# Kernel tuning notes

Hardware: AMD Instinct MI355X
Metric: run time of the kernel (lower is better)

## Reference

```python
import jax, jax.numpy as jnp
import numpy as np


def _shift(x, axis, d):
    # value at voxel p becomes x[p + d*e_axis], zero outside the grid
    n = x.shape[axis]
    zero = jnp.zeros_like(jax.lax.slice_in_dim(x, 0, 1, axis=axis))
    if d > 0:
        return jnp.concatenate([jax.lax.slice_in_dim(x, 1, n, axis=axis), zero], axis=axis)
    return jnp.concatenate([zero, jax.lax.slice_in_dim(x, 0, n - 1, axis=axis)], axis=axis)


def _forward(coords, instance_gt, S, num_scales):
    # InputLayer mode=4: average features of duplicate coords.
    # features = [instance+1, 1]; averaging duplicates of [v,1] gives [mean(v), 1].
    inst = instance_gt.astype(jnp.float32) + 1.0
    c = coords.astype(jnp.int32)
    flat = (c[:, 0] * S + c[:, 1]) * S + c[:, 2]
    ssum = jnp.zeros(S * S * S, jnp.float32).at[flat].add(inst)
    cnt = jnp.zeros(S * S * S, jnp.float32).at[flat].add(1.0)
    val = (ssum / jnp.maximum(cnt, 1.0)).reshape(S, S, S)   # mean label per active voxel, 0 if inactive
    act = (cnt > 0).astype(jnp.float32).reshape(S, S, S)    # active-site mask
    outs = []
    for scale in range(num_scales):
        if scale == 0:
            v, a = val, act
        else:
            f = 2 ** scale
            Ss = S // f
            # scn AveragePooling divides by pool volume; features[:, :1]/count then
            # renormalizes -> mean of val over ACTIVE fine voxels in the block.
            vsum = val.reshape(Ss, f, Ss, f, Ss, f).sum(axis=(1, 3, 5))
            asum = act.reshape(Ss, f, Ss, f, Ss, f).sum(axis=(1, 3, 5))
            a = (asum > 0).astype(jnp.float32)
            v = vsum / jnp.maximum(asum, 1.0)
        va = v * a
        feats = []
        masks = []
        # one-hot submanifold conv kernel offsets (4,22,10,16,12,14) = (-x,+x,-y,+y,-z,+z)
        for axis in range(3):
            for d in (-1, 1):
                sh = _shift(va, axis, d)                      # neighbor value, 0 if neighbor inactive
                feats.append((jnp.abs(sh - v) < 0.01).astype(jnp.float32))
                masks.append((sh > 0).astype(jnp.float32))
        # submanifold conv is only defined at active sites -> mask by a
        out = jnp.stack(feats + masks, axis=-1) * a[..., None]  # [Ss,Ss,Ss,12]
        outs.append(out.reshape(-1, 12))
    return jnp.concatenate(outs, axis=0)


def setup_inputs() -> dict:
    key = jax.random.key(0)
    k1, k2 = jax.random.split(key)
    N, S = 4_000_000, 128
    coords = jax.random.randint(k1, (N, 3), 0, S, dtype=jnp.int32)
    instance_gt = jax.random.randint(k2, (N,), 0, 50).astype(jnp.float32)
    return {"coords": coords, "instance_gt": instance_gt, "inputScale": S, "numScales": 6}


def reference(coords, instance_gt, inputScale, numScales):
    return _forward(coords, instance_gt, inputScale, numScales)
```

## Files before the change

kernel.cpp:

```cpp
#include <hip/hip_runtime.h>

#define GS3 2097152
#define NS1 262144
#define NS2 32768
#define NS3 4096
#define NS4 512
#define NS5 64
#define NSALL 299584

#define OB1 25165824
#define OB2 28311552
#define OB3 28704768
#define OB4 28753920
#define OB5 28760064

#define NREG 512
#define RVOX 4096
#define PPB  8192
#define RPT  (PPB / 256)
#define CAPB 64


__global__ __launch_bounds__(256) void bin_kernel(
    const int* __restrict__ coords, const float* __restrict__ inst,
    unsigned int* __restrict__ counts, unsigned int* __restrict__ bins, int N) {
  __shared__ unsigned srec[PPB];
  __shared__ unsigned hist[NREG];
  __shared__ unsigned lofs[NREG];
  __shared__ unsigned part[256];
  __shared__ unsigned total_sh;
  unsigned vrec[RPT];
  int tid = threadIdx.x;
  int bid = blockIdx.x;
  int start = bid * PPB;
  for (int j = tid; j < NREG; j += 256) hist[j] = 0;
  __syncthreads();
#pragma unroll
  for (int j = 0; j < RPT; j++) {
    int i = start + j * 256 + tid;
    unsigned v = 0xFFFFFFFFu;
    if (i < N) {
      int x = coords[3 * i + 0];
      int y = coords[3 * i + 1];
      int z = coords[3 * i + 2];
      unsigned lab = (unsigned)inst[i] + 1u;
      unsigned r = (((unsigned)x >> 1) << 3) | ((unsigned)y >> 4);
      unsigned l = (((unsigned)x & 1) << 11) | (((unsigned)y & 15) << 7) | (unsigned)z;
      v = (r << 18) | (l << 6) | lab;
      atomicAdd(&hist[r], 1u);
    }
    vrec[j] = v;
  }
  __syncthreads();
  unsigned ha = hist[2 * tid], hb = hist[2 * tid + 1];
  counts[(size_t)bid * NREG + 2 * tid]     = ha < CAPB ? ha : CAPB;
  counts[(size_t)bid * NREG + 2 * tid + 1] = hb < CAPB ? hb : CAPB;
  part[tid] = ha + hb;
  __syncthreads();
  for (int o = 1; o < 256; o <<= 1) {
    unsigned v = part[tid];
    unsigned add = (tid >= o) ? part[tid - o] : 0u;
    __syncthreads();
    part[tid] = v + add;
    __syncthreads();
  }
  unsigned inc = part[tid];
  unsigned ex = inc - (ha + hb);
  lofs[2 * tid] = ex;
  lofs[2 * tid + 1] = ex + ha;
  if (tid == 255) total_sh = inc;
  __syncthreads();
  for (int j = tid; j < NREG; j += 256) hist[j] = 0;
  __syncthreads();
#pragma unroll
  for (int j = 0; j < RPT; j++) {
    unsigned v = vrec[j];
    if (v != 0xFFFFFFFFu) {
      unsigned r = v >> 18;
      unsigned pos = lofs[r] + atomicAdd(&hist[r], 1u);
      srec[pos] = v;
    }
  }
  __syncthreads();
  unsigned total = total_sh;
  size_t bbase = (size_t)bid * NREG * CAPB;
  for (unsigned j = tid; j < total; j += 256) {
    unsigned v = srec[j];
    unsigned r = v >> 18;
    unsigned p = j - lofs[r];
    if (p < CAPB) bins[bbase + r * CAPB + p] = v & 0x3FFFFu;
  }
}

__global__ __launch_bounds__(256) void build_pool_kernel(
    const unsigned int* __restrict__ counts, const unsigned int* __restrict__ bins,
    unsigned int* __restrict__ P,
    double* __restrict__ vs1, double* __restrict__ as1, int nchunks) {
  __shared__ unsigned grid[RVOX];
  int r = blockIdx.x;
  int tid = threadIdx.x;
  for (int j = tid; j < RVOX; j += 256) grid[j] = 0;
  __syncthreads();
  for (int b = tid; b < nchunks; b += 256) {
    int cb = (int)counts[(size_t)b * NREG + r];
    const unsigned* src = bins + ((size_t)b * NREG + r) * CAPB;
    for (int k = 0; k < cb; k++) {
      unsigned v = src[k];
      atomicAdd(&grid[v >> 6], (1u << 20) | (v & 63u));
    }
  }
  __syncthreads();
  int X = r >> 3, yo = r & 7;
  unsigned pbase = ((unsigned)(2 * X) << 14) | ((unsigned)yo << 11);
  for (int j = tid; j < RVOX; j += 256) {
    P[pbase + ((j >> 11) << 14) + (j & 0x7FF)] = grid[j];
  }
  for (int c = tid; c < 512; c += 256) {
    int yl = c >> 6, Z = c & 63;
    double vs = 0.0, as = 0.0;
#pragma unroll
    for (int dx = 0; dx < 2; dx++)
#pragma unroll
      for (int dy = 0; dy < 2; dy++)
#pragma unroll
        for (int dz = 0; dz < 2; dz++) {
          int j = (dx << 11) | ((2 * yl + dy) << 7) | (2 * Z + dz);
          unsigned pk = grid[j];
          unsigned cc = pk >> 20;
          if (cc) {
            vs += (double)(pk & 0xFFFFFu) / (double)cc;
            as += 1.0;
          }
        }
    int q = (X << 12) | (((yo << 3) + yl) << 6) | Z;
    vs1[q] = vs;
    as1[q] = as;
  }
}

__global__ __launch_bounds__(256) void poolRest_kernel(
    const double* __restrict__ vs1, const double* __restrict__ as1,
    double* __restrict__ vs2, double* __restrict__ as2,
    double* __restrict__ vs3, double* __restrict__ as3,
    double* __restrict__ vs4, double* __restrict__ as4,
    double* __restrict__ vs5, double* __restrict__ as5) {
  int t = blockIdx.x * blockDim.x + threadIdx.x;

  if (t < NS2) {
    int q = t;
    int X = q >> 10, Y = (q >> 5) & 31, Z = q & 31;
    double vs = 0.0, as = 0.0;
#pragma unroll
    for (int dx = 0; dx < 2; dx++)
#pragma unroll
      for (int dy = 0; dy < 2; dy++)
#pragma unroll
        for (int dz = 0; dz < 2; dz++) {
          int p = ((((X << 1) + dx) << 12) + (((Y << 1) + dy) << 6) + ((Z << 1) + dz));
          vs += vs1[p];
          as += as1[p];
        }
    vs2[q] = vs;
    as2[q] = as;
    return;
  }
  t -= NS2;
  if (t < NS3) {
    int q = t;
    int X = q >> 8, Y = (q >> 4) & 15, Z = q & 15;
    double vs = 0.0, as = 0.0;
    for (int dx = 0; dx < 4; dx++)
      for (int dy = 0; dy < 4; dy++)
#pragma unroll
        for (int dz = 0; dz < 4; dz++) {
          int p = ((((X << 2) + dx) << 12) + (((Y << 2) + dy) << 6) + ((Z << 2) + dz));
          vs += vs1[p];
          as += as1[p];
        }
    vs3[q] = vs;
    as3[q] = as;
    return;
  }
  t -= NS3;
  if (t < NS4 * 64) {
    int w = t >> 6, lane = t & 63;
    int X = w >> 6, Y = (w >> 3) & 7, Z = w & 7;
    double vs = 0.0, as = 0.0;
#pragma unroll
    for (int j = 0; j < 8; j++) {
      int c = lane * 8 + j;
      int dx = c >> 6, dy = (c >> 3) & 7, dz = c & 7;
      int p = ((((X << 3) + dx) << 12) + (((Y << 3) + dy) << 6) + ((Z << 3) + dz));
      vs += vs1[p];
      as += as1[p];
    }
    for (int o = 32; o > 0; o >>= 1) {
      vs += __shfl_down(vs, o, 64);
      as += __shfl_down(as, o, 64);
    }
    if (lane == 0) { vs4[w] = vs; as4[w] = as; }
    return;
  }
  t -= NS4 * 64;
  if (t < NS5 * 64) {
    int w = t >> 6, lane = t & 63;
    int X = w >> 4, Y = (w >> 2) & 3, Z = w & 3;
    double vs = 0.0, as = 0.0;
    for (int j = 0; j < 64; j++) {
      int c = lane * 64 + j;
      int dx = c >> 8, dy = (c >> 4) & 15, dz = c & 15;
      int p = ((((X << 4) + dx) << 12) + (((Y << 4) + dy) << 6) + ((Z << 4) + dz));
      vs += vs1[p];
      as += as1[p];
    }
    for (int o = 32; o > 0; o >>= 1) {
      vs += __shfl_down(vs, o, 64);
      as += __shfl_down(as, o, 64);
    }
    if (lane == 0) { vs5[w] = vs; as5[w] = as; }
  }
}

__global__ __launch_bounds__(256) void out_kernel(
    const unsigned int* __restrict__ P,
    const double* __restrict__ vs1, const double* __restrict__ as1,
    const double* __restrict__ vs2, const double* __restrict__ as2,
    const double* __restrict__ vs3, const double* __restrict__ as3,
    const double* __restrict__ vs4, const double* __restrict__ as4,
    const double* __restrict__ vs5, const double* __restrict__ as5,
    float* __restrict__ out) {
  int p = blockIdx.x * blockDim.x + threadIdx.x;
  if (p < GS3) {
    unsigned pk = P[p];
    int cc = (int)(pk >> 20);
    float4 r0 = {0.f, 0.f, 0.f, 0.f}, r1 = r0, r2 = r0;
    if (cc) {
      int sc = (int)(pk & 0xFFFFFu);
      int x = p >> 14, y = (p >> 7) & 127, z = p & 127;
      const int off[6] = {-(1 << 14), (1 << 14), -(1 << 7), (1 << 7), -1, 1};
      const bool inb[6] = {x > 0, x < 127, y > 0, y < 127, z > 0, z < 127};
      float f[6], m[6];
#pragma unroll
      for (int k = 0; k < 6; k++) {
        int sn = 0, cn = 0;
        if (inb[k]) {
          unsigned pn = P[p + off[k]];
          cn = (int)(pn >> 20);
          sn = (int)(pn & 0xFFFFFu);
        }
        if (cn) {
          long long d = (long long)sn * cc - (long long)sc * cn;
          if (d < 0) d = -d;
          f[k] = (100ll * d < (long long)cn * cc) ? 1.f : 0.f;
          m[k] = 1.f;
        } else {
          f[k] = 0.f;
          m[k] = 0.f;
        }
      }
      r0 = {f[0], f[1], f[2], f[3]};
      r1 = {f[4], f[5], m[0], m[1]};
      r2 = {m[2], m[3], m[4], m[5]};
    }
    float4* o = (float4*)(out + 12ll * p);
    o[0] = r0; o[1] = r1; o[2] = r2;
    return;
  }
  int t = p - GS3;
  const double *vs, *as;
  int ls, q;
  long long obase;
  if (t < NS1) { q = t; vs = vs1; as = as1; ls = 6; obase = OB1; }
  else if (t < NS1 + NS2) { q = t - NS1; vs = vs2; as = as2; ls = 5; obase = OB2; }
  else if (t < NS1 + NS2 + NS3) { q = t - NS1 - NS2; vs = vs3; as = as3; ls = 4; obase = OB3; }
  else if (t < NS1 + NS2 + NS3 + NS4) { q = t - NS1 - NS2 - NS3; vs = vs4; as = as4; ls = 3; obase = OB4; }
  else if (t < NSALL) { q = t - NS1 - NS2 - NS3 - NS4; vs = vs5; as = as5; ls = 2; obase = OB5; }
  else return;

  int Ss = 1 << ls;
  int X = q >> (2 * ls), Y = (q >> ls) & (Ss - 1), Z = q & (Ss - 1);
  double ac = as[q];
  float4 r0 = {0.f, 0.f, 0.f, 0.f}, r1 = r0, r2 = r0;
  if (ac > 0.0) {
    double vc = vs[q] / ac;
    const int off[6] = {-(Ss * Ss), Ss * Ss, -Ss, Ss, -1, 1};
    const bool inb[6] = {X > 0, X < Ss - 1, Y > 0, Y < Ss - 1, Z > 0, Z < Ss - 1};
    float f[6], m[6];
#pragma unroll
    for (int k = 0; k < 6; k++) {
      double van = 0.0;
      if (inb[k]) {
        double an = as[q + off[k]];
        if (an > 0.0) van = vs[q + off[k]] / an;
      }
      f[k] = (fabs(van - vc) < 0.01) ? 1.f : 0.f;
      m[k] = (van > 0.0) ? 1.f : 0.f;
    }
    r0 = {f[0], f[1], f[2], f[3]};
    r1 = {f[4], f[5], m[0], m[1]};
    r2 = {m[2], m[3], m[4], m[5]};
  }
  float4* o = (float4*)(out + obase + 12ll * q);
  o[0] = r0; o[1] = r1; o[2] = r2;
}

extern "C" void kernel_launch(void* const* d_in, const int* in_sizes, int n_in,
                              void* d_out, int out_size, void* d_ws, size_t ws_size,
                              hipStream_t stream) {
  const int* coords = (const int*)d_in[0];
  const float* inst = (const float*)d_in[1];
  int N = in_sizes[1];
  float* out = (float*)d_out;
  int nchunks = (N + PPB - 1) / PPB;

  char* base = (char*)d_ws;
  unsigned int* P = (unsigned int*)base;
  double* vs1 = (double*)(base + 8388608);
  double* as1 = vs1 + NS1;
  double* vs2 = as1 + NS1; double* as2 = vs2 + NS2;
  double* vs3 = as2 + NS2; double* as3 = vs3 + NS3;
  double* vs4 = as3 + NS3; double* as4 = vs4 + NS4;
  double* vs5 = as4 + NS4; double* as5 = vs5 + NS5;
  size_t counts_off = 13182976;
  unsigned int* counts = (unsigned int*)(base + counts_off);
  size_t bins_off = counts_off + ((size_t)nchunks * NREG * 4 + 1023) / 1024 * 1024;
  unsigned int* bins = (unsigned int*)(base + bins_off);
  size_t need = bins_off + (size_t)nchunks * NREG * CAPB * 4;
  if (ws_size < need) return;

  bin_kernel<<<nchunks, 256, 0, stream>>>(coords, inst, counts, bins, N);
  build_pool_kernel<<<NREG, 256, 0, stream>>>(counts, bins, P, vs1, as1, nchunks);
  poolRest_kernel<<<(NS2 + NS3 + NS4 * 64 + NS5 * 64 + 255) / 256, 256, 0, stream>>>(
      vs1, as1, vs2, as2, vs3, as3, vs4, as4, vs5, as5);
  out_kernel<<<(GS3 + NSALL + 255) / 256, 256, 0, stream>>>(
      P, vs1, as1, vs2, as2, vs3, as3, vs4, as4, vs5, as5, out);
}
```

Before: 86.41 us.

## Fuse coarse pooling scales into output kernel, recomputing neighbor block sums

Drops the separate poolRest kernel and the intermediate vs2..vs5 buffers. Each coarse-scale output thread, or wave for the two coarsest scales, now sums the scale-1 pooled values for its own block and its six neighbors, then writes the 12 features directly. This removes one kernel launch and a global round trip. In exchange every pooled block is reduced up to seven times, which is extra reads of vs1/as1 and longer per-thread loops at scales 2 and 3.

After: 159.0 us. +84.0%, slower.

```diff
diff --git a/kernel.cpp b/kernel.cpp
--- a/kernel.cpp
+++ b/kernel.cpp
@@ -6,7 +6,6 @@
 #define NS3 4096
 #define NS4 512
 #define NS5 64
-#define NSALL 299584
 
 #define OB1 25165824
 #define OB2 28311552
@@ -19,6 +18,13 @@
 #define PPB  8192
 #define RPT  (PPB / 256)
 #define CAPB 64
+
+#define T1 (GS3)
+#define T2 (T1 + NS1)
+#define T3 (T2 + NS2)
+#define T4 (T3 + NS3)
+#define T5 (T4 + NS4 * 64)
+#define TEND (T5 + NS5 * 64)
 
 
 __global__ __launch_bounds__(256) void bin_kernel(
@@ -138,96 +144,104 @@
   }
 }
 
-__global__ __launch_bounds__(256) void poolRest_kernel(
+__device__ __forceinline__ void writeOut12(float* dst, const float* f, const float* m) {
+  float4 r0 = {f[0], f[1], f[2], f[3]};
+  float4 r1 = {f[4], f[5], m[0], m[1]};
+  float4 r2 = {m[2], m[3], m[4], m[5]};
+  float4* o = (float4*)dst;
+  o[0] = r0; o[1] = r1; o[2] = r2;
+}
+
+__device__ __forceinline__ void coarse_thread(
     const double* __restrict__ vs1, const double* __restrict__ as1,
-    double* __restrict__ vs2, double* __restrict__ as2,
-    double* __restrict__ vs3, double* __restrict__ as3,
-    double* __restrict__ vs4, double* __restrict__ as4,
-    double* __restrict__ vs5, double* __restrict__ as5) {
-  int t = blockIdx.x * blockDim.x + threadIdx.x;
-
-  if (t < NS2) {
-    int q = t;
-    int X = q >> 10, Y = (q >> 5) & 31, Z = q & 31;
-    double vs = 0.0, as = 0.0;
-#pragma unroll
-    for (int dx = 0; dx < 2; dx++)
-#pragma unroll
-      for (int dy = 0; dy < 2; dy++)
-#pragma unroll
-        for (int dz = 0; dz < 2; dz++) {
-          int p = ((((X << 1) + dx) << 12) + (((Y << 1) + dy) << 6) + ((Z << 1) + dz));
-          vs += vs1[p];
-          as += as1[p];
-        }
-    vs2[q] = vs;
-    as2[q] = as;
-    return;
-  }
-  t -= NS2;
-  if (t < NS3) {
-    int q = t;
-    int X = q >> 8, Y = (q >> 4) & 15, Z = q & 15;
-    double vs = 0.0, as = 0.0;
-    for (int dx = 0; dx < 4; dx++)
-      for (int dy = 0; dy < 4; dy++)
-#pragma unroll
-        for (int dz = 0; dz < 4; dz++) {
-          int p = ((((X << 2) + dx) << 12) + (((Y << 2) + dy) << 6) + ((Z << 2) + dz));
-          vs += vs1[p];
-          as += as1[p];
-        }
-    vs3[q] = vs;
-    as3[q] = as;
-    return;
-  }
-  t -= NS3;
-  if (t < NS4 * 64) {
-    int w = t >> 6, lane = t & 63;
-    int X = w >> 6, Y = (w >> 3) & 7, Z = w & 7;
-    double vs = 0.0, as = 0.0;
-#pragma unroll
-    for (int j = 0; j < 8; j++) {
-      int c = lane * 8 + j;
-      int dx = c >> 6, dy = (c >> 3) & 7, dz = c & 7;
-      int p = ((((X << 3) + dx) << 12) + (((Y << 3) + dy) << 6) + ((Z << 3) + dz));
-      vs += vs1[p];
-      as += as1[p];
-    }
+    float* __restrict__ out, int q, int lg, int lc, long long obase) {
+  int G = 1 << lg, C = 1 << lc;
+  int X = q >> (2 * lg), Y = (q >> lg) & (G - 1), Z = q & (G - 1);
+  const int cx[7] = {X, X - 1, X + 1, X, X, X, X};
+  const int cy[7] = {Y, Y, Y, Y - 1, Y + 1, Y, Y};
+  const int cz[7] = {Z, Z, Z, Z, Z, Z - 1, Z + 1};
+  double vsum[7], asum[7];
+#pragma unroll
+  for (int c = 0; c < 7; c++) {
+    vsum[c] = 0.0; asum[c] = 0.0;
+    if (cx[c] < 0 || cx[c] >= G || cy[c] < 0 || cy[c] >= G || cz[c] < 0 || cz[c] >= G)
+      continue;
+    int bx = cx[c] << lc, by = cy[c] << lc, bz = cz[c] << lc;
+    for (int dx = 0; dx < C; dx++)
+      for (int dy = 0; dy < C; dy++)
+        for (int dz = 0; dz < C; dz++) {
+          int p1 = ((bx + dx) << 12) | ((by + dy) << 6) | (bz + dz);
+          vsum[c] += vs1[p1];
+          asum[c] += as1[p1];
+        }
+  }
+  float f[6], m[6];
+  if (asum[0] > 0.0) {
+    double vc = vsum[0] / asum[0];
+#pragma unroll
+    for (int k = 0; k < 6; k++) {
+      double van = (asum[k + 1] > 0.0) ? vsum[k + 1] / asum[k + 1] : 0.0;
+      f[k] = (fabs(van - vc) < 0.01) ? 1.f : 0.f;
+      m[k] = (van > 0.0) ? 1.f : 0.f;
+    }
+  } else {
+#pragma unroll
+    for (int k = 0; k < 6; k++) { f[k] = 0.f; m[k] = 0.f; }
+  }
+  writeOut12(out + obase + 12ll * q, f, m);
+}
+
+__device__ __forceinline__ void coarse_wave(
+    const double* __restrict__ vs1, const double* __restrict__ as1,
+    float* __restrict__ out, int t, int lg, int lc, long long obase) {
+  int w = t >> 6, lane = t & 63;
+  int G = 1 << lg, C = 1 << lc, vol = C * C * C;
+  int X = w >> (2 * lg), Y = (w >> lg) & (G - 1), Z = w & (G - 1);
+  const int cx[7] = {X, X - 1, X + 1, X, X, X, X};
+  const int cy[7] = {Y, Y, Y, Y - 1, Y + 1, Y, Y};
+  const int cz[7] = {Z, Z, Z, Z, Z, Z - 1, Z + 1};
+  double vsum[7], asum[7];
+#pragma unroll
+  for (int c = 0; c < 7; c++) {
+    vsum[c] = 0.0; asum[c] = 0.0;
+    if (cx[c] < 0 || cx[c] >= G || cy[c] < 0 || cy[c] >= G || cz[c] < 0 || cz[c] >= G)
+      continue;
+    int bx = cx[c] << lc, by = cy[c] << lc, bz = cz[c] << lc;
+    for (int ch = lane; ch < vol; ch += 64) {
+      int dx = ch >> (2 * lc), dy = (ch >> lc) & (C - 1), dz = ch & (C - 1);
+      int p1 = ((bx + dx) << 12) | ((by + dy) << 6) | (bz + dz);
+      vsum[c] += vs1[p1];
+      asum[c] += as1[p1];
+    }
+  }
+#pragma unroll
+  for (int c = 0; c < 7; c++) {
     for (int o = 32; o > 0; o >>= 1) {
-      vs += __shfl_down(vs, o, 64);
-      as += __shfl_down(as, o, 64);
-    }
-    if (lane == 0) { vs4[w] = vs; as4[w] = as; }
-    return;
-  }
-  t -= NS4 * 64;
-  if (t < NS5 * 64) {
-    int w = t >> 6, lane = t & 63;
-    int X = w >> 4, Y = (w >> 2) & 3, Z = w & 3;
-    double vs = 0.0, as = 0.0;
-    for (int j = 0; j < 64; j++) {
-      int c = lane * 64 + j;
-      int dx = c >> 8, dy = (c >> 4) & 15, dz = c & 15;
-      int p = ((((X << 4) + dx) << 12) + (((Y << 4) + dy) << 6) + ((Z << 4) + dz));
-      vs += vs1[p];
-      as += as1[p];
-    }
-    for (int o = 32; o > 0; o >>= 1) {
-      vs += __shfl_down(vs, o, 64);
-      as += __shfl_down(as, o, 64);
-    }
-    if (lane == 0) { vs5[w] = vs; as5[w] = as; }
+      vsum[c] += __shfl_down(vsum[c], o, 64);
+      asum[c] += __shfl_down(asum[c], o, 64);
+    }
+  }
+  if (lane == 0) {
+    float f[6], m[6];
+    if (asum[0] > 0.0) {
+      double vc = vsum[0] / asum[0];
+#pragma unroll
+      for (int k = 0; k < 6; k++) {
+        double van = (asum[k + 1] > 0.0) ? vsum[k + 1] / asum[k + 1] : 0.0;
+        f[k] = (fabs(van - vc) < 0.01) ? 1.f : 0.f;
+        m[k] = (van > 0.0) ? 1.f : 0.f;
+      }
+    } else {
+#pragma unroll
+      for (int k = 0; k < 6; k++) { f[k] = 0.f; m[k] = 0.f; }
+    }
+    writeOut12(out + obase + 12ll * w, f, m);
   }
 }
 
 __global__ __launch_bounds__(256) void out_kernel(
     const unsigned int* __restrict__ P,
     const double* __restrict__ vs1, const double* __restrict__ as1,
-    const double* __restrict__ vs2, const double* __restrict__ as2,
-    const double* __restrict__ vs3, const double* __restrict__ as3,
-    const double* __restrict__ vs4, const double* __restrict__ as4,
-    const double* __restrict__ vs5, const double* __restrict__ as5,
     float* __restrict__ out) {
   int p = blockIdx.x * blockDim.x + threadIdx.x;
   if (p < GS3) {
@@ -266,42 +280,36 @@
     o[0] = r0; o[1] = r1; o[2] = r2;
     return;
   }
-  int t = p - GS3;
-  const double *vs, *as;
-  int ls, q;
-  long long obase;
-  if (t < NS1) { q = t; vs = vs1; as = as1; ls = 6; obase = OB1; }
-  else if (t < NS1 + NS2) { q = t - NS1; vs = vs2; as = as2; ls = 5; obase = OB2; }
-  else if (t < NS1 + NS2 + NS3) { q = t - NS1 - NS2; vs = vs3; as = as3; ls = 4; obase = OB3; }
-  else if (t < NS1 + NS2 + NS3 + NS4) { q = t - NS1 - NS2 - NS3; vs = vs4; as = as4; ls = 3; obase = OB4; }
-  else if (t < NSALL) { q = t - NS1 - NS2 - NS3 - NS4; vs = vs5; as = as5; ls = 2; obase = OB5; }
-  else return;
-
-  int Ss = 1 << ls;
-  int X = q >> (2 * ls), Y = (q >> ls) & (Ss - 1), Z = q & (Ss - 1);
-  double ac = as[q];
-  float4 r0 = {0.f, 0.f, 0.f, 0.f}, r1 = r0, r2 = r0;
-  if (ac > 0.0) {
-    double vc = vs[q] / ac;
-    const int off[6] = {-(Ss * Ss), Ss * Ss, -Ss, Ss, -1, 1};
-    const bool inb[6] = {X > 0, X < Ss - 1, Y > 0, Y < Ss - 1, Z > 0, Z < Ss - 1};
+  if (p < T2) {
+    int q = p - T1;
+    int X = q >> 12, Y = (q >> 6) & 63, Z = q & 63;
+    double ac = as1[q];
     float f[6], m[6];
-#pragma unroll
-    for (int k = 0; k < 6; k++) {
-      double van = 0.0;
-      if (inb[k]) {
-        double an = as[q + off[k]];
-        if (an > 0.0) van = vs[q + off[k]] / an;
+    if (ac > 0.0) {
+      double vc = vs1[q] / ac;
+      const int off[6] = {-4096, 4096, -64, 64, -1, 1};
+      const bool inb[6] = {X > 0, X < 63, Y > 0, Y < 63, Z > 0, Z < 63};
+#pragma unroll
+      for (int k = 0; k < 6; k++) {
+        double van = 0.0;
+        if (inb[k]) {
+          double an = as1[q + off[k]];
+          if (an > 0.0) van = vs1[q + off[k]] / an;
+        }
+        f[k] = (fabs(van - vc) < 0.01) ? 1.f : 0.f;
+        m[k] = (van > 0.0) ? 1.f : 0.f;
       }
-      f[k] = (fabs(van - vc) < 0.01) ? 1.f : 0.f;
-      m[k] = (van > 0.0) ? 1.f : 0.f;
-    }
-    r0 = {f[0], f[1], f[2], f[3]};
-    r1 = {f[4], f[5], m[0], m[1]};
-    r2 = {m[2], m[3], m[4], m[5]};
-  }
-  float4* o = (float4*)(out + obase + 12ll * q);
-  o[0] = r0; o[1] = r1; o[2] = r2;
+    } else {
+#pragma unroll
+      for (int k = 0; k < 6; k++) { f[k] = 0.f; m[k] = 0.f; }
+    }
+    writeOut12(out + OB1 + 12ll * q, f, m);
+    return;
+  }
+  if (p < T3) { coarse_thread(vs1, as1, out, p - T2, 5, 1, OB2); return; }
+  if (p < T4) { coarse_thread(vs1, as1, out, p - T3, 4, 2, OB3); return; }
+  if (p < T5) { coarse_wave(vs1, as1, out, p - T4, 3, 3, OB4); return; }
+  if (p < TEND) { coarse_wave(vs1, as1, out, p - T5, 2, 4, OB5); }
 }
 
 extern "C" void kernel_launch(void* const* d_in, const int* in_sizes, int n_in,
@@ -317,10 +325,6 @@
   unsigned int* P = (unsigned int*)base;
   double* vs1 = (double*)(base + 8388608);
   double* as1 = vs1 + NS1;
-  double* vs2 = as1 + NS1; double* as2 = vs2 + NS2;
-  double* vs3 = as2 + NS2; double* as3 = vs3 + NS3;
-  double* vs4 = as3 + NS3; double* as4 = vs4 + NS4;
-  double* vs5 = as4 + NS4; double* as5 = vs5 + NS5;
   size_t counts_off = 13182976;
   unsigned int* counts = (unsigned int*)(base + counts_off);
   size_t bins_off = counts_off + ((size_t)nchunks * NREG * 4 + 1023) / 1024 * 1024;
@@ -330,8 +334,5 @@
 
   bin_kernel<<<nchunks, 256, 0, stream>>>(coords, inst, counts, bins, N);
   build_pool_kernel<<<NREG, 256, 0, stream>>>(counts, bins, P, vs1, as1, nchunks);
-  poolRest_kernel<<<(NS2 + NS3 + NS4 * 64 + NS5 * 64 + 255) / 256, 256, 0, stream>>>(
-      vs1, as1, vs2, as2, vs3, as3, vs4, as4, vs5, as5);
-  out_kernel<<<(GS3 + NSALL + 255) / 256, 256, 0, stream>>>(
-      P, vs1, as1, vs2, as2, vs3, as3, vs4, as4, vs5, as5, out);
-}
+  out_kernel<<<TEND / 256, 256, 0, stream>>>(P, vs1, as1, out);
+}
```
